# Kernel optimization log

Hardware: AMD Instinct MI355X
Metric: run time of the kernel (lower is better)

## Reference

```python
import jax, jax.numpy as jnp
import numpy as np

N_OUT = 100000 - 1  # 99999, as hard-coded in the torch module
LEAK = 0.01         # torch LeakyReLU default slope


def setup_inputs() -> dict:
    key = jax.random.key(0)
    k1, k2, k3, k4, k5 = jax.random.split(key, 5)
    B, D = 512, 512
    H = D // 2
    x = jax.random.normal(k1, (B, D), dtype=jnp.float32)
    # torch.nn.Linear-style init scale ~ 1/sqrt(fan_in)
    w2 = jax.random.normal(k2, (H, D), dtype=jnp.float32) / np.sqrt(D)
    b2 = jax.random.normal(k3, (H,), dtype=jnp.float32) / np.sqrt(D)
    w3 = jax.random.normal(k4, (55, H), dtype=jnp.float32) / np.sqrt(H)
    b3 = jax.random.normal(k5, (55,), dtype=jnp.float32) / np.sqrt(H)
    return {"x": x, "w2": w2, "b2": b2, "w3": w3, "b3": b3}


def _digit_tables():
    # Static integer tables for i in [0, N_OUT).
    i = np.arange(N_OUT, dtype=np.int32)
    ndig = ((i >= 10).astype(np.int32) + (i >= 100) + (i >= 1000) + (i >= 10000)).astype(np.int32)
    ndig[0] = 1  # special case in the original code: i==0 -> n=1
    return jnp.asarray(i), jnp.asarray(ndig)


def reference(x, w2, b2, w3, b3):
    # tiny MLP (batched; equivalent to the per-sample torch loop)
    h = x @ w2.T + b2
    h = jnp.where(h >= 0, h, LEAK * h)          # LeakyReLU
    z = h @ w3.T + b3                            # [B, 55]
    p_len = jax.nn.softmax(z[:, :5], axis=-1)    # length distribution (5)
    p_dig = jax.nn.softmax(z[:, 5:].reshape(-1, 5, 10), axis=-1)  # 5 digit groups of 10
    x3 = jnp.concatenate([p_len, p_dig.reshape(-1, 50)], axis=-1)  # [B, 55]

    i, ndig = _digit_tables()                    # [N], [N]
    out = jnp.take(x3, ndig, axis=1)             # lead factor x3[k, n_i] -> [B, N]
    # Multiply the first n_i digit probabilities (original drops the last digit).
    for j in range(4):                           # max usable digits: n<=4
        expo = jnp.maximum(ndig - j, 0)
        d = (i // jnp.power(10, expo)) % 10      # j-th most significant digit
        idx = 5 + d + 10 * j                     # index into x3 digit groups
        factor = jnp.take(x3, idx, axis=1)       # [B, N]
        valid = (j < ndig)[None, :]
        out = out * jnp.where(valid, factor, 1.0)
    return out
```

## Files before the change

kernel.cpp:

```cpp
#include <hip/hip_runtime.h>


#define BATCH 512
#define DIM   512
#define HID   256
#define NCLS  55
#define NOUT  99999
#define LEAK  0.01f

__global__ __launch_bounds__(512) void fused_mlp_expand(
    const float* __restrict__ x,  const float* __restrict__ w2,
    const float* __restrict__ b2, const float* __restrict__ w3,
    const float* __restrict__ b3, float* __restrict__ out) {
    __shared__ float xs[DIM];
    __shared__ float hs[HID];
    __shared__ float x3s[NCLS];
    __shared__ float AB[100];
    __shared__ float CD[100];
    __shared__ float VS[10004];

    const int tid  = threadIdx.x;
    const int k    = blockIdx.x;
    const int wave = tid >> 6;
    const int lane = tid & 63;

    xs[tid] = x[(size_t)k * DIM + tid];
    __syncthreads();

    {
        float4 xv0 = ((const float4*)xs)[lane];
        float4 xv1 = ((const float4*)xs)[lane + 64];
        float  acc = 0.f;
#pragma unroll 4
        for (int t = 0; t < 32; ++t) {
            const int n = wave * 32 + t;
            const float4* w2r = (const float4*)(w2 + (size_t)n * DIM);
            float4 a = w2r[lane];
            float4 b = w2r[lane + 64];
            float s = a.x * xv0.x + a.y * xv0.y + a.z * xv0.z + a.w * xv0.w
                    + b.x * xv1.x + b.y * xv1.y + b.z * xv1.z + b.w * xv1.w;
#pragma unroll
            for (int off = 1; off < 64; off <<= 1) s += __shfl_xor(s, off, 64);
            if (lane == t) acc = s;
        }
        if (lane < 32) {
            float hv = acc + b2[wave * 32 + lane];
            hs[wave * 32 + lane] = (hv >= 0.f) ? hv : LEAK * hv;
        }
    }
    __syncthreads();

    {
        float4 hv = ((const float4*)hs)[lane];
        for (int o = wave; o < NCLS; o += 8) {
            const float4* w3r = (const float4*)(w3 + (size_t)o * HID);
            float4 w = w3r[lane];
            float s = w.x * hv.x + w.y * hv.y + w.z * hv.z + w.w * hv.w;
#pragma unroll
            for (int off = 1; off < 64; off <<= 1) s += __shfl_xor(s, off, 64);
            if (lane == 0) x3s[o] = s + b3[o];
        }
    }
    __syncthreads();

    if (tid < 6) {
        int off = (tid == 0) ? 0 : 5 + 10 * (tid - 1);
        int len = (tid == 0) ? 5 : 10;
        float m = -1e30f;
        for (int u = 0; u < len; ++u) m = fmaxf(m, x3s[off + u]);
        float s = 0.f;
        for (int u = 0; u < len; ++u) {
            float e = __expf(x3s[off + u] - m);
            x3s[off + u] = e;
            s += e;
        }
        float inv = 1.f / s;
        for (int u = 0; u < len; ++u) x3s[off + u] *= inv;
    }
    __syncthreads();

    if (tid < 100) {
        int hi = tid / 10, lo = tid % 10;
        AB[tid] = x3s[5 + hi] * x3s[15 + lo];
        CD[tid] = x3s[25 + hi] * x3s[35 + lo];
    }
    __syncthreads();

    {
        const float A10 = x3s[0];
        const float L1 = x3s[1], L2 = x3s[2], L3 = x3s[3], L4 = x3s[4];
        for (int j = tid; j < 10000; j += 512) {
            unsigned ju = (unsigned)j;
            float v;
            if (ju >= 1000u)      { unsigned q = ju / 100u; v = L4 * AB[q] * CD[ju - q * 100u]; }
            else if (ju >= 100u)  { unsigned q = ju / 10u;  v = L3 * AB[q] * x3s[25 + (ju - q * 10u)]; }
            else if (ju >= 10u)   { v = L2 * AB[ju]; }
            else                  { v = (ju == 0u) ? A10 : L1 * x3s[5 + ju]; }
            VS[j] = v;
        }
    }
    __syncthreads();

    const float  pz = x3s[1] * x3s[5];
    const size_t rb = (size_t)k * NOUT;
    const unsigned h     = (unsigned)((4u - (unsigned)(rb & 3)) & 3u);
    const unsigned ng    = ((unsigned)NOUT - h) >> 2;
    const unsigned tail0 = h + (ng << 2);

    if (tid < (int)h) {
        unsigned e = (unsigned)tid;
        out[rb + e] = (e == 0u) ? pz : VS[0];
    }
    if (tid < (int)((unsigned)NOUT - tail0)) {
        unsigned e = tail0 + (unsigned)tid;
        out[rb + e] = VS[e / 10u];
    }

    float4* outv = (float4*)(out + rb + h);
    for (unsigned g = tid; g < ng; g += 512) {
        unsigned e   = h + (g << 2);
        unsigned j   = e / 10u;
        unsigned rem = e - j * 10u;
        float v0 = VS[j];
        float v1 = VS[j + 1];
        float4 v;
        v.x = (e == 0u)  ? pz : v0;
        v.y = (rem < 9u) ? v0 : v1;
        v.z = (rem < 8u) ? v0 : v1;
        v.w = (rem < 7u) ? v0 : v1;
        outv[g] = v;
    }
}

extern "C" void kernel_launch(void* const* d_in, const int* in_sizes, int n_in,
                              void* d_out, int out_size, void* d_ws, size_t ws_size,
                              hipStream_t stream) {
    const float* x  = (const float*)d_in[0];
    const float* w2 = (const float*)d_in[1];
    const float* b2 = (const float*)d_in[2];
    const float* w3 = (const float*)d_in[3];
    const float* b3 = (const float*)d_in[4];
    float* out = (float*)d_out;

    fused_mlp_expand<<<BATCH, 512, 0, stream>>>(x, w2, b2, w3, b3, out);
}
```

Measured before the change: 230.2 us.

## Split fused kernel into MLP and sliced expansion kernels for more parallelism

```diff
diff --git a/kernel.cpp b/kernel.cpp
--- a/kernel.cpp
+++ b/kernel.cpp
@@ -7,17 +7,16 @@
 #define NCLS  55
 #define NOUT  99999
 #define LEAK  0.01f
+#define SLICE_EL 25000
+#define SLICE_J  2500
 
-__global__ __launch_bounds__(512) void fused_mlp_expand(
+__global__ __launch_bounds__(512) void mlp_x3_kernel(
     const float* __restrict__ x,  const float* __restrict__ w2,
     const float* __restrict__ b2, const float* __restrict__ w3,
-    const float* __restrict__ b3, float* __restrict__ out) {
+    const float* __restrict__ b3, float* __restrict__ x3out) {
     __shared__ float xs[DIM];
     __shared__ float hs[HID];
     __shared__ float x3s[NCLS];
-    __shared__ float AB[100];
-    __shared__ float CD[100];
-    __shared__ float VS[10004];
 
     const int tid  = threadIdx.x;
     const int k    = blockIdx.x;
@@ -79,6 +78,24 @@
     }
     __syncthreads();
 
+    if (tid < NCLS) x3out[k * NCLS + tid] = x3s[tid];
+}
+
+__global__ __launch_bounds__(256) void expand_kernel(
+    const float* __restrict__ x3g, float* __restrict__ out) {
+    __shared__ float x3s[NCLS];
+    __shared__ float AB[100];
+    __shared__ float CD[100];
+    __shared__ float VSs[SLICE_J + 4];
+
+    const int tid = threadIdx.x;
+    const int b   = blockIdx.x;
+    const int k   = b >> 2;
+    const int s   = b & 3;
+
+    if (tid < NCLS) x3s[tid] = x3g[k * NCLS + tid];
+    __syncthreads();
+
     if (tid < 100) {
         int hi = tid / 10, lo = tid % 10;
         AB[tid] = x3s[5 + hi] * x3s[15 + lo];
@@ -89,42 +106,45 @@
     {
         const float A10 = x3s[0];
         const float L1 = x3s[1], L2 = x3s[2], L3 = x3s[3], L4 = x3s[4];
-        for (int j = tid; j < 10000; j += 512) {
-            unsigned ju = (unsigned)j;
+        for (int jj = tid; jj <= SLICE_J; jj += 256) {
+            unsigned j = (unsigned)(jj + SLICE_J * s);
+            if (j > 9999u) j = 9999u;
             float v;
-            if (ju >= 1000u)      { unsigned q = ju / 100u; v = L4 * AB[q] * CD[ju - q * 100u]; }
-            else if (ju >= 100u)  { unsigned q = ju / 10u;  v = L3 * AB[q] * x3s[25 + (ju - q * 10u)]; }
-            else if (ju >= 10u)   { v = L2 * AB[ju]; }
-            else                  { v = (ju == 0u) ? A10 : L1 * x3s[5 + ju]; }
-            VS[j] = v;
+            if (j >= 1000u)      { unsigned q = j / 100u; v = L4 * AB[q] * CD[j - q * 100u]; }
+            else if (j >= 100u)  { unsigned q = j / 10u;  v = L3 * AB[q] * x3s[25 + (j - q * 10u)]; }
+            else if (j >= 10u)   { v = L2 * AB[j]; }
+            else                 { v = (j == 0u) ? A10 : L1 * x3s[5 + j]; }
+            VSs[jj] = v;
         }
     }
     __syncthreads();
 
-    const float  pz = x3s[1] * x3s[5];
-    const size_t rb = (size_t)k * NOUT;
-    const unsigned h     = (unsigned)((4u - (unsigned)(rb & 3)) & 3u);
-    const unsigned ng    = ((unsigned)NOUT - h) >> 2;
+    const bool  z0   = (s == 0);
+    const float pz   = x3s[1] * x3s[5];
+    const unsigned n_el = (s == 3) ? 24999u : 25000u;
+    const size_t gbase  = (size_t)k * NOUT + (unsigned)(SLICE_EL * s);
+    const unsigned h     = (unsigned)((4u - (unsigned)(gbase & 3u)) & 3u);
+    const unsigned ng    = (n_el - h) >> 2;
     const unsigned tail0 = h + (ng << 2);
 
     if (tid < (int)h) {
-        unsigned e = (unsigned)tid;
-        out[rb + e] = (e == 0u) ? pz : VS[0];
+        unsigned el = (unsigned)tid;
+        out[gbase + el] = (z0 && el == 0u) ? pz : VSs[0];
     }
-    if (tid < (int)((unsigned)NOUT - tail0)) {
-        unsigned e = tail0 + (unsigned)tid;
-        out[rb + e] = VS[e / 10u];
+    if (tid < (int)(n_el - tail0)) {
+        unsigned el = tail0 + (unsigned)tid;
+        out[gbase + el] = VSs[el / 10u];
     }
 
-    float4* outv = (float4*)(out + rb + h);
-    for (unsigned g = tid; g < ng; g += 512) {
-        unsigned e   = h + (g << 2);
-        unsigned j   = e / 10u;
-        unsigned rem = e - j * 10u;
-        float v0 = VS[j];
-        float v1 = VS[j + 1];
+    float4* outv = (float4*)(out + gbase + h);
+    for (unsigned g = tid; g < ng; g += 256) {
+        unsigned el  = h + (g << 2);
+        unsigned jj  = el / 10u;
+        unsigned rem = el - jj * 10u;
+        float v0 = VSs[jj];
+        float v1 = VSs[jj + 1];
         float4 v;
-        v.x = (e == 0u)  ? pz : v0;
+        v.x = (z0 && el == 0u) ? pz : v0;
         v.y = (rem < 9u) ? v0 : v1;
         v.z = (rem < 8u) ? v0 : v1;
         v.w = (rem < 7u) ? v0 : v1;
@@ -141,6 +161,8 @@
     const float* w3 = (const float*)d_in[3];
     const float* b3 = (const float*)d_in[4];
     float* out = (float*)d_out;
+    float* x3  = (float*)d_ws;
 
-    fused_mlp_expand<<<BATCH, 512, 0, stream>>>(x, w2, b2, w3, b3, out);
+    mlp_x3_kernel<<<BATCH, 512, 0, stream>>>(x, w2, b2, w3, b3, x3);
+    expand_kernel<<<BATCH * 4, 256, 0, stream>>>(x3, out);
 }
```

After: 231.7 us. Within noise of the previous version (+0.6%).
